# Kernel tuning notes

Measured on AMD Instinct MI355X. Metric: run time of the kernel, lower is better.

## Reference

```python
import jax
import jax.numpy as jnp
from jax import lax
import numpy as np

B, CIN, COUT, RANK, K, H, W = 16, 256, 256, 64, 3, 112, 112
PAD = 1


def setup_inputs() -> dict:
    key = jax.random.key(0)
    k1, k2, k3, k4, k5 = jax.random.split(key, 5)
    x = jax.random.normal(k1, (B, CIN, H, W), dtype=jnp.float32)
    # head: `rank` stacked 1x1 conv weights, each [COUT, CIN]
    w_head = jax.random.normal(k2, (RANK, COUT, CIN), dtype=jnp.float32) * 0.05
    # body: Conv2d(COUT -> RANK, kernel (K,1)), OIHW layout
    w_body = jax.random.normal(k3, (RANK, COUT, K, 1), dtype=jnp.float32) * 0.05
    # tail: Conv2d(RANK -> COUT, kernel (1,K)), OIHW layout, with bias
    w_tail = jax.random.normal(k4, (COUT, RANK, 1, K), dtype=jnp.float32) * 0.05
    b_tail = jax.random.normal(k5, (COUT,), dtype=jnp.float32) * 0.05
    return {"x": x, "w_head": w_head, "w_body": w_body, "w_tail": w_tail, "b_tail": b_tail}


_DN = lax.conv_dimension_numbers((B, CIN, H, W), (COUT, CIN, 1, 1), ("NCHW", "OIHW", "NCHW"))


def reference(x, w_head, w_body, w_tail, b_tail):
    # Sum of rank 1x1 convs over the same input == one 1x1 conv with summed
    # weights (conv is linear in the weight) — same math, one pass.
    w_sum = w_head.sum(axis=0)                      # [COUT, CIN]
    y = jnp.einsum("bihw,oi->bohw", x, w_sum)       # [B, COUT, H, W]
    # body: (K,1) conv, stride (1,1), padding (PAD, 0)
    y = lax.conv_general_dilated(y, w_body, window_strides=(1, 1),
                                 padding=((PAD, PAD), (0, 0)),
                                 dimension_numbers=_DN)  # [B, RANK, H, W]
    # tail: (1,K) conv, stride (1,1), padding (0, PAD), plus bias
    y = lax.conv_general_dilated(y, w_tail, window_strides=(1, 1),
                                 padding=((0, 0), (PAD, PAD)),
                                 dimension_numbers=_DN)  # [B, COUT, H, W]
    return y + b_tail[None, :, None, None]
```

## Files before the change

### kernel.cpp

```cpp
#include <hip/hip_runtime.h>
#include <stdint.h>

#define CIN 256
#define COUT 256
#define RANK 64
#define H_ 112
#define W_ 112
#define HW_ (112*112)

typedef short bf16x8 __attribute__((ext_vector_type(8)));
typedef float f32x4 __attribute__((ext_vector_type(4)));

__device__ __forceinline__ unsigned rne2(float a, float b){
  unsigned ua = __builtin_bit_cast(unsigned, a);
  unsigned ub = __builtin_bit_cast(unsigned, b);
  ua += 0x7FFFu + ((ua >> 16) & 1u);
  ub += 0x7FFFu + ((ub >> 16) & 1u);
  return (ua >> 16) | (ub & 0xFFFF0000u);
}
__device__ __forceinline__ unsigned short rne1(float a){
  unsigned ua = __builtin_bit_cast(unsigned, a);
  ua += 0x7FFFu + ((ua >> 16) & 1u);
  return (unsigned short)(ua >> 16);
}

__global__ __launch_bounds__(256) void k_wsum(const float* __restrict__ wh,
                                              float* __restrict__ wsum){
  int o = blockIdx.x, i = threadIdx.x;
  float s = 0.f;
  for (int k = 0; k < RANK; ++k) s += wh[(k*COUT + o)*CIN + i];
  wsum[o*CIN + i] = s;
}

__global__ __launch_bounds__(256) void k_pre2(const float* __restrict__ wb,
                                              const float* __restrict__ wsum,
                                              unsigned short* __restrict__ weff,
                                              const float* __restrict__ wt,
                                              unsigned short* __restrict__ wtp){
  const int tid = threadIdx.x;
  if (blockIdx.x < 192){
    int bid = blockIdx.x;
    int dh = bid >> 6, r = bid & 63;
    float s = 0.f;
    for (int o = 0; o < COUT; ++o)
      s += wb[(r*COUT + o)*3 + dh] * wsum[o*CIN + tid];
    weff[bid*CIN + tid] = rne1(s);
  } else {
    int o = blockIdx.x - 192;
    if (tid < 192){
      int dw = tid >> 6, r = tid & 63;
      wtp[o*192 + tid] = rne1(wt[(o*RANK + r)*3 + dw]);
    }
  }
}

__global__ __launch_bounds__(256,2) void k_all(const float* __restrict__ x,
                                               const unsigned short* __restrict__ weff,
                                               const unsigned short* __restrict__ wtp,
                                               const float* __restrict__ bias,
                                               float* __restrict__ out,
                                               unsigned cpx){
  __shared__ alignas(16) unsigned short lds[16416];
  const int tid  = threadIdx.x;
  const int wid  = tid >> 6, lane = tid & 63, g = lane >> 4, l15 = lane & 15;
  const unsigned orig = blockIdx.x;
  const unsigned wg   = (orig & 7u)*cpx + (orig >> 3);
  const int bb   = wg / 56, hb = wg % 56;
  const int h0   = hb*2;
  const int hloc = wid >> 1, rhalf = wid & 1;

  const int q_st  = lane & 3, cpair = lane >> 2;
  const int g_st  = cpair >> 2, cp3 = cpair & 3;
  const int grow  = h0 - 1 + wid;
  const bool rok  = (grow >= 0) && (grow < H_);
  const float* xrow = x + ((size_t)bb*CIN + cpair*2)*HW_ + (size_t)(rok ? grow : 0)*W_;
  unsigned char* const stg = (unsigned char*)lds;

  f32x4 acc[2][7];
  #pragma unroll
  for (int a = 0; a < 2; ++a)
    #pragma unroll
    for (int b = 0; b < 7; ++b) acc[a][b] = (f32x4){0.f,0.f,0.f,0.f};

  f32x4 av[7], bv[7];
  auto LOADS = [&](int i0){
    const float* pa = xrow + (size_t)i0*32*HW_;
    #pragma unroll
    for (int j = 0; j < 7; ++j){
      const int w0 = 16*j + q_st*4;
      if (rok){
        av[j] = *(const f32x4*)(pa + w0);
        bv[j] = *(const f32x4*)(pa + HW_ + w0);
      } else {
        av[j] = (f32x4){0.f,0.f,0.f,0.f};
        bv[j] = (f32x4){0.f,0.f,0.f,0.f};
      }
    }
  };
  auto WRITE = [&](){
    unsigned char* base = stg + wid*7168 + g_st*1792 + cp3*4;
    #pragma unroll
    for (int j = 0; j < 7; ++j){
      const int w0 = 16*j + q_st*4;
      #pragma unroll
      for (int k = 0; k < 4; ++k){
        unsigned pk = rne2(av[j][k], bv[j][k]);
        *(unsigned*)(base + (unsigned)(((w0 + k) ^ (g_st & 3))*16)) = pk;
      }
    }
  };
  auto MSTEP = [&](int i0){
    #pragma unroll
    for (int dh = 0; dh < 3; ++dh){
      const unsigned short* ab = weff + (size_t)(dh*64 + rhalf*32 + l15)*CIN + i0*32 + g*8;
      bf16x8 af0 = *(const bf16x8*)(ab);
      bf16x8 af1 = *(const bf16x8*)(ab + 16*CIN);
      const unsigned char* rowb = stg + (hloc + dh)*7168 + g*1792;
      #pragma unroll
      for (int wt = 0; wt < 7; ++wt){
        const int w = wt*16 + l15;
        bf16x8 bfv = *(const bf16x8*)(rowb + ((w ^ (g & 3))*16));
        acc[0][wt] = __builtin_amdgcn_mfma_f32_16x16x32_bf16(af0, bfv, acc[0][wt], 0, 0, 0);
        acc[1][wt] = __builtin_amdgcn_mfma_f32_16x16x32_bf16(af1, bfv, acc[1][wt], 0, 0, 0);
      }
    }
  };

  LOADS(0);
  for (int t = 0; t < 8; ++t){
    __syncthreads();
    WRITE();
    if (t < 7) LOADS(t+1);
    __syncthreads();
    MSTEP(t);
  }
  __syncthreads();

  unsigned short* y2b = lds;
  if (tid < 32){
    int hh = tid >> 4, wsel = (tid >> 3) & 1, rq = tid & 7;
    *(uint4*)(y2b + hh*8208 + (wsel ? 113 : 0)*72 + rq*8) = (uint4){0,0,0,0};
  }
  #pragma unroll
  for (int wt = 0; wt < 7; ++wt){
    #pragma unroll
    for (int rt = 0; rt < 2; ++rt){
      unsigned lo = rne2(acc[rt][wt][0], acc[rt][wt][1]);
      unsigned hi = rne2(acc[rt][wt][2], acc[rt][wt][3]);
      uint2 st; st.x = lo; st.y = hi;
      *(uint2*)(y2b + hloc*8208 + (wt*16 + l15 + 1)*72 + rhalf*32 + rt*16 + g*4) = st;
    }
  }
  __syncthreads();

  const int h = h0 + hloc;
  #pragma unroll
  for (int opass = 0; opass < 4; ++opass){
    const int obase = rhalf*128 + opass*32;
    f32x4 a2[2][7];
    #pragma unroll
    for (int a = 0; a < 2; ++a)
      #pragma unroll
      for (int b = 0; b < 7; ++b) a2[a][b] = (f32x4){0.f,0.f,0.f,0.f};

    #pragma unroll
    for (int s = 0; s < 6; ++s){
      bf16x8 afc[2];
      const unsigned short* ab = wtp + (size_t)(obase + l15)*192 + s*32 + g*8;
      #pragma unroll
      for (int rt = 0; rt < 2; ++rt)
        afc[rt] = *(const bf16x8*)(ab + rt*16*192);
      const unsigned short* qb = y2b + hloc*8208 + (l15 + (s >> 1))*72 + (s & 1)*32 + g*8;
      #pragma unroll
      for (int wt = 0; wt < 7; ++wt){
        bf16x8 bvv = *(const bf16x8*)(qb + wt*16*72);
        #pragma unroll
        for (int rt = 0; rt < 2; ++rt)
          a2[rt][wt] = __builtin_amdgcn_mfma_f32_16x16x32_bf16(afc[rt], bvv, a2[rt][wt], 0, 0, 0);
      }
    }

    float* ob = out + ((size_t)(bb*COUT) + obase)*HW_ + h*W_;
    #pragma unroll
    for (int rt = 0; rt < 2; ++rt){
      #pragma unroll
      for (int ii = 0; ii < 4; ++ii){
        float bvv = bias[obase + rt*16 + g*4 + ii];
        #pragma unroll
        for (int wt = 0; wt < 7; ++wt)
          ob[(size_t)(rt*16 + g*4 + ii)*HW_ + wt*16 + l15] = a2[rt][wt][ii] + bvv;
      }
    }
  }
}

extern "C" void kernel_launch(void* const* d_in, const int* in_sizes, int n_in,
                              void* d_out, int out_size, void* d_ws, size_t ws_size,
                              hipStream_t stream) {
  const float* x      = (const float*)d_in[0];
  const float* w_head = (const float*)d_in[1];
  const float* w_body = (const float*)d_in[2];
  const float* w_tail = (const float*)d_in[3];
  const float* b_tail = (const float*)d_in[4];
  float* out = (float*)d_out;
  char* ws = (char*)d_ws;

  float*          wsum = (float*)ws;
  unsigned short* weff = (unsigned short*)(ws + 262144);
  unsigned short* wtp  = (unsigned short*)(ws + 360448);

  k_wsum<<<256, 256, 0, stream>>>(w_head, wsum);
  k_pre2<<<448, 256, 0, stream>>>(w_body, wsum, weff, w_tail, wtp);
  k_all <<<896, 256, 0, stream>>>(x, weff, wtp, b_tail, out, 112u);
}
```

Baseline: 162.4 us.

## Double-buffer global loads with manual waitcnt, hardware bf16 pack, new LDS swizzle

Prefetches the input tile and weff fragments two stages ahead into register double buffers, using explicit s_waitcnt vmcnt and raw s_barrier in place of __syncthreads so global loads overlap the MFMA steps. It replaces the software round-to-nearest-even bf16 packing with the v_cvt_pk_bf16_f32 instruction and changes the LDS XOR swizzle so address math is simpler and bank conflicts are reduced. In exchange it uses more registers, which may hurt occupancy, and the vmcnt count is hand-tuned, which is fragile if the compiler reorders or merges loads.

```diff
diff --git a/kernel.cpp b/kernel.cpp
--- a/kernel.cpp
+++ b/kernel.cpp
@@ -11,17 +11,15 @@
 typedef short bf16x8 __attribute__((ext_vector_type(8)));
 typedef float f32x4 __attribute__((ext_vector_type(4)));
 
-__device__ __forceinline__ unsigned rne2(float a, float b){
-  unsigned ua = __builtin_bit_cast(unsigned, a);
-  unsigned ub = __builtin_bit_cast(unsigned, b);
-  ua += 0x7FFFu + ((ua >> 16) & 1u);
-  ub += 0x7FFFu + ((ub >> 16) & 1u);
-  return (ua >> 16) | (ub & 0xFFFF0000u);
-}
 __device__ __forceinline__ unsigned short rne1(float a){
   unsigned ua = __builtin_bit_cast(unsigned, a);
   ua += 0x7FFFu + ((ua >> 16) & 1u);
   return (unsigned short)(ua >> 16);
+}
+__device__ __forceinline__ unsigned cvtpk(float a, float b){
+  unsigned r;
+  asm("v_cvt_pk_bf16_f32 %0, %1, %2" : "=v"(r) : "v"(a), "v"(b));
+  return r;
 }
 
 __global__ __launch_bounds__(256) void k_wsum(const float* __restrict__ wh,
@@ -69,12 +67,14 @@
   const int h0   = hb*2;
   const int hloc = wid >> 1, rhalf = wid & 1;
 
-  const int q_st  = lane & 3, cpair = lane >> 2;
-  const int g_st  = cpair >> 2, cp3 = cpair & 3;
-  const int grow  = h0 - 1 + wid;
-  const bool rok  = (grow >= 0) && (grow < H_);
+  const int q_st = lane & 3, cpair = lane >> 2;
+  const int g_st = cpair >> 2, cp3 = cpair & 3;
+  const int grow = h0 - 1 + wid;
+  const bool rok = (grow >= 0) && (grow < H_);
   const float* xrow = x + ((size_t)bb*CIN + cpair*2)*HW_ + (size_t)(rok ? grow : 0)*W_;
   unsigned char* const stg = (unsigned char*)lds;
+  const int cxor = (g_st ^ q_st) & 3;
+  const int lxor = (l15 ^ (g & 3) ^ ((l15 >> 2) & 3));
 
   f32x4 acc[2][7];
   #pragma unroll
@@ -82,59 +82,69 @@
     #pragma unroll
     for (int b = 0; b < 7; ++b) acc[a][b] = (f32x4){0.f,0.f,0.f,0.f};
 
-  f32x4 av[7], bv[7];
-  auto LOADS = [&](int i0){
-    const float* pa = xrow + (size_t)i0*32*HW_;
+  f32x4  xa[2][7], xb[2][7];
+  bf16x8 afp[2][3][2];
+
+  auto ISSUE = [&](int t){
+    const int s = t & 1;
+    #pragma unroll
+    for (int dh = 0; dh < 3; ++dh){
+      const unsigned short* ab = weff + (size_t)(dh*64 + rhalf*32 + l15)*CIN + t*32 + g*8;
+      afp[s][dh][0] = *(const bf16x8*)(ab);
+      afp[s][dh][1] = *(const bf16x8*)(ab + 16*CIN);
+    }
+    const float* pa = xrow + (size_t)t*32*HW_;
     #pragma unroll
     for (int j = 0; j < 7; ++j){
       const int w0 = 16*j + q_st*4;
       if (rok){
-        av[j] = *(const f32x4*)(pa + w0);
-        bv[j] = *(const f32x4*)(pa + HW_ + w0);
+        xa[s][j] = *(const f32x4*)(pa + w0);
+        xb[s][j] = *(const f32x4*)(pa + HW_ + w0);
       } else {
-        av[j] = (f32x4){0.f,0.f,0.f,0.f};
-        bv[j] = (f32x4){0.f,0.f,0.f,0.f};
+        xa[s][j] = (f32x4){0.f,0.f,0.f,0.f};
+        xb[s][j] = (f32x4){0.f,0.f,0.f,0.f};
       }
     }
   };
-  auto WRITE = [&](){
+  auto WRITE = [&](int t){
+    const int s = t & 1;
     unsigned char* base = stg + wid*7168 + g_st*1792 + cp3*4;
     #pragma unroll
     for (int j = 0; j < 7; ++j){
       const int w0 = 16*j + q_st*4;
       #pragma unroll
       for (int k = 0; k < 4; ++k){
-        unsigned pk = rne2(av[j][k], bv[j][k]);
-        *(unsigned*)(base + (unsigned)(((w0 + k) ^ (g_st & 3))*16)) = pk;
+        unsigned pk = cvtpk(xa[s][j][k], xb[s][j][k]);
+        *(unsigned*)(base + (unsigned)(w0*16) + (unsigned)((k ^ cxor) << 4)) = pk;
       }
     }
   };
-  auto MSTEP = [&](int i0){
+  auto MSTEP = [&](int t){
+    const int s = t & 1;
     #pragma unroll
     for (int dh = 0; dh < 3; ++dh){
-      const unsigned short* ab = weff + (size_t)(dh*64 + rhalf*32 + l15)*CIN + i0*32 + g*8;
-      bf16x8 af0 = *(const bf16x8*)(ab);
-      bf16x8 af1 = *(const bf16x8*)(ab + 16*CIN);
-      const unsigned char* rowb = stg + (hloc + dh)*7168 + g*1792;
+      const unsigned char* rowb = stg + (hloc + dh)*7168 + g*1792 + lxor*16;
       #pragma unroll
       for (int wt = 0; wt < 7; ++wt){
-        const int w = wt*16 + l15;
-        bf16x8 bfv = *(const bf16x8*)(rowb + ((w ^ (g & 3))*16));
-        acc[0][wt] = __builtin_amdgcn_mfma_f32_16x16x32_bf16(af0, bfv, acc[0][wt], 0, 0, 0);
-        acc[1][wt] = __builtin_amdgcn_mfma_f32_16x16x32_bf16(af1, bfv, acc[1][wt], 0, 0, 0);
+        bf16x8 bfv = *(const bf16x8*)(rowb + wt*256);
+        acc[0][wt] = __builtin_amdgcn_mfma_f32_16x16x32_bf16(afp[s][dh][0], bfv, acc[0][wt], 0, 0, 0);
+        acc[1][wt] = __builtin_amdgcn_mfma_f32_16x16x32_bf16(afp[s][dh][1], bfv, acc[1][wt], 0, 0, 0);
       }
     }
   };
 
-  LOADS(0);
+  ISSUE(0); ISSUE(1);
+  #pragma unroll
   for (int t = 0; t < 8; ++t){
-    __syncthreads();
-    WRITE();
-    if (t < 7) LOADS(t+1);
-    __syncthreads();
+    if (t < 7) asm volatile("s_waitcnt vmcnt(20)" ::: "memory");
+    else       asm volatile("s_waitcnt vmcnt(0)"  ::: "memory");
+    WRITE(t);
+    asm volatile("s_waitcnt lgkmcnt(0)" ::: "memory");
+    __builtin_amdgcn_s_barrier();
     MSTEP(t);
-  }
-  __syncthreads();
+    if (t < 6) ISSUE(t + 2);
+    __builtin_amdgcn_s_barrier();
+  }
 
   unsigned short* y2b = lds;
   if (tid < 32){
@@ -145,9 +155,9 @@
   for (int wt = 0; wt < 7; ++wt){
     #pragma unroll
     for (int rt = 0; rt < 2; ++rt){
-      unsigned lo = rne2(acc[rt][wt][0], acc[rt][wt][1]);
-      unsigned hi = rne2(acc[rt][wt][2], acc[rt][wt][3]);
-      uint2 st; st.x = lo; st.y = hi;
+      uint2 st;
+      st.x = cvtpk(acc[rt][wt][0], acc[rt][wt][1]);
+      st.y = cvtpk(acc[rt][wt][2], acc[rt][wt][3]);
       *(uint2*)(y2b + hloc*8208 + (wt*16 + l15 + 1)*72 + rhalf*32 + rt*16 + g*4) = st;
     }
   }
```

Result: no change. 162.0 us (-0.2%).
